# Kernel optimization log

Measured on AMD Instinct MI355X. Metric: run time of the kernel, lower is better.

The kernel has to match this reference:

```python
import jax, jax.numpy as jnp
import numpy as np

B, D, H, W = 32, 64, 64, 64
K = 1024

def setup_inputs() -> dict:
    key = jax.random.key(0)
    k1, k2 = jax.random.split(key)
    x = jax.random.normal(k1, (B, D, H, W), dtype=jnp.float32)
    # nn.Parameter(torch.rand(embeddings_dim, num_embeddings)) -> uniform [0,1)
    emb = jax.random.uniform(k2, (D, K), dtype=jnp.float32)
    return {"x": x, "emb": emb}


def reference(x, emb):
    # x: [B, D, H, W], emb: [D, K]
    b, d, h, w = x.shape
    xf = jnp.transpose(x, (0, 2, 3, 1)).reshape(-1, d)  # [N, D], N = B*H*W
    # squared L2 distance (same argmin as torch.norm(.,2) distance)
    d2 = (
        jnp.sum(xf * xf, axis=-1, keepdims=True)
        - 2.0 * (xf @ emb)
        + jnp.sum(emb * emb, axis=0)
    )  # [N, K]
    argmin = jnp.argmin(d2, axis=-1)  # [N]
    # gather codebook vectors: emb.T[argmin] -> [N, D]
    q = jnp.take(emb.T, argmin, axis=0)
    result = jnp.transpose(q.reshape(b, h, w, d), (0, 3, 1, 2))  # [B, D, H, W]
    return result, argmin.reshape(b, h, w)
```

## Files before the change

kernel.cpp:

```cpp
#include <hip/hip_runtime.h>


using half8 = __attribute__((ext_vector_type(8))) _Float16;
using half4 = __attribute__((ext_vector_type(4))) _Float16;
using f32x4 = __attribute__((ext_vector_type(4))) float;

#define XPITCH 72

__global__ void prep_kernel(const float* __restrict__ emb,
                            float* __restrict__ e2,
                            _Float16* __restrict__ eTh,
                            _Float16* __restrict__ eTl) {
    int k = blockIdx.x * 64 + threadIdx.x;
    float s = 0.f;
#pragma unroll
    for (int c = 0; c < 8; ++c) {
        half8 hv, lv;
#pragma unroll
        for (int j = 0; j < 8; ++j) {
            float v = emb[(c * 8 + j) * 1024 + k];
            s = fmaf(v, v, s);
            _Float16 h = (_Float16)v;
            hv[j] = h;
            lv[j] = (_Float16)(v - (float)h);
        }
        *(half8*)(eTh + k * 64 + c * 8) = hv;
        *(half8*)(eTl + k * 64 + c * 8) = lv;
    }
    e2[k] = s;
}

__launch_bounds__(256)
__global__ void vq_kernel(const float* __restrict__ x,
                          const _Float16* __restrict__ eTh,
                          const _Float16* __restrict__ eTl,
                          const float* __restrict__ e2,
                          const float* __restrict__ emb,
                          float* __restrict__ outq,
                          float* __restrict__ outidx) {
    __shared__ _Float16 sxh[64 * XPITCH];
    __shared__ _Float16 sxl[64 * XPITCH];
    __shared__ float rbest[256];
    __shared__ int   ridx[256];
    __shared__ int   samin[64];

    const int tx = threadIdx.x;
    const int n0 = blockIdx.x * 64;
    const int bb = n0 >> 12;
    const int hw = n0 & 4095;
    const float* xbase = x + bb * 262144 + hw;

    {
        const int p  = tx & 63;
        const int dg = (tx >> 6) << 2;
#pragma unroll
        for (int it = 0; it < 4; ++it) {
            int d0 = it * 16 + dg;
            float v0 = xbase[(d0 + 0) * 4096 + p];
            float v1 = xbase[(d0 + 1) * 4096 + p];
            float v2 = xbase[(d0 + 2) * 4096 + p];
            float v3 = xbase[(d0 + 3) * 4096 + p];
            _Float16 h0 = (_Float16)v0, h1 = (_Float16)v1,
                     h2 = (_Float16)v2, h3 = (_Float16)v3;
            half4 hv = {h0, h1, h2, h3};
            half4 lv = {(_Float16)(v0 - (float)h0), (_Float16)(v1 - (float)h1),
                        (_Float16)(v2 - (float)h2), (_Float16)(v3 - (float)h3)};
            *(half4*)(sxh + p * XPITCH + d0) = hv;
            *(half4*)(sxl + p * XPITCH + d0) = lv;
        }
    }
    __syncthreads();

    const int lane = tx & 63;
    const int w    = tx >> 6;
    const int r16  = lane & 15;
    const int q    = lane >> 4;

    half8 ah[4][2], al[4][2];
#pragma unroll
    for (int mt = 0; mt < 4; ++mt)
#pragma unroll
        for (int s = 0; s < 2; ++s) {
            ah[mt][s] = *(const half8*)(sxh + (mt * 16 + r16) * XPITCH + s * 32 + q * 8);
            al[mt][s] = *(const half8*)(sxl + (mt * 16 + r16) * XPITCH + s * 32 + q * 8);
        }
#pragma unroll
    for (int mt = 0; mt < 4; ++mt)
#pragma unroll
        for (int s = 0; s < 2; ++s) {
            asm volatile("" : "+v"(ah[mt][s]));
            asm volatile("" : "+v"(al[mt][s]));
        }

    float best[16];
    int   bestk[16];
#pragma unroll
    for (int i = 0; i < 16; ++i) { best[i] = 3.4e38f; bestk[i] = 0; }

    const int kw = w << 8;
    const _Float16* bhbase = eTh + (kw + r16) * 64 + q * 8;
    const _Float16* blbase = eTl + (kw + r16) * 64 + q * 8;
    const float*    e2base = e2 + kw + r16;

    half8 pbh0, pbh1, pbl0, pbl1; float pe2;
    half8 qbh0, qbh1, qbl0, qbl1; float qe2;

#define LOADSET(BH0, BH1, BL0, BL1, E2V, TT)                                  \
    {                                                                         \
        const int off_ = (TT) << 10;                \
        BH0 = *(const half8*)(bhbase + off_);                                 \
        BH1 = *(const half8*)(bhbase + off_ + 32);                            \
        BL0 = *(const half8*)(blbase + off_);                                 \
        BL1 = *(const half8*)(blbase + off_ + 32);                            \
        E2V = e2base[(TT) << 4];                                              \
    }

#define COMPUTE(BH0, BH1, BL0, BL1, E2V, TT)                                  \
    {                                                                         \
        const int klc_ = kw + ((TT) << 4) + r16;                              \
        _Pragma("unroll")                                                     \
        for (int mt = 0; mt < 4; ++mt) {                                      \
            f32x4 a = {0.f, 0.f, 0.f, 0.f};                                   \
            a = __builtin_amdgcn_mfma_f32_16x16x32_f16(al[mt][0], BL0, a, 0, 0, 0); \
            a = __builtin_amdgcn_mfma_f32_16x16x32_f16(al[mt][1], BL1, a, 0, 0, 0); \
            a = __builtin_amdgcn_mfma_f32_16x16x32_f16(al[mt][0], BH0, a, 0, 0, 0); \
            a = __builtin_amdgcn_mfma_f32_16x16x32_f16(al[mt][1], BH1, a, 0, 0, 0); \
            a = __builtin_amdgcn_mfma_f32_16x16x32_f16(ah[mt][0], BL0, a, 0, 0, 0); \
            a = __builtin_amdgcn_mfma_f32_16x16x32_f16(ah[mt][1], BL1, a, 0, 0, 0); \
            a = __builtin_amdgcn_mfma_f32_16x16x32_f16(ah[mt][0], BH0, a, 0, 0, 0); \
            a = __builtin_amdgcn_mfma_f32_16x16x32_f16(ah[mt][1], BH1, a, 0, 0, 0); \
            _Pragma("unroll")                                                 \
            for (int rr = 0; rr < 4; ++rr) {                                  \
                float dist_ = fmaf(-2.f, a[rr], E2V);                         \
                int i_ = mt * 4 + rr;                                         \
                if (dist_ < best[i_]) { best[i_] = dist_; bestk[i_] = klc_; } \
            }                                                                 \
        }                                                                     \
    }

    LOADSET(pbh0, pbh1, pbl0, pbl1, pe2, 0);
#pragma unroll 1
    for (int t = 0; t < 16; t += 2) {
        LOADSET(qbh0, qbh1, qbl0, qbl1, qe2, t + 1);
        COMPUTE(pbh0, pbh1, pbl0, pbl1, pe2, t);
        LOADSET(pbh0, pbh1, pbl0, pbl1, pe2, (t + 2) & 15);
        COMPUTE(qbh0, qbh1, qbl0, qbl1, qe2, t + 1);
    }

#pragma unroll
    for (int i = 0; i < 16; ++i) {
        float bv = best[i];
        int   bk = bestk[i];
#pragma unroll
        for (int m = 1; m < 16; m <<= 1) {
            float ov = __shfl_xor(bv, m, 64);
            int   ok = __shfl_xor(bk, m, 64);
            if (ov < bv || (ov == bv && ok < bk)) { bv = ov; bk = ok; }
        }
        best[i] = bv;
        bestk[i] = bk;
    }
    if (r16 == 0) {
#pragma unroll
        for (int mt = 0; mt < 4; ++mt)
#pragma unroll
            for (int rr = 0; rr < 4; ++rr) {
                int p = mt * 16 + q * 4 + rr;
                rbest[w * 64 + p] = best[mt * 4 + rr];
                ridx[w * 64 + p]  = bestk[mt * 4 + rr];
            }
    }
    __syncthreads();

    if (tx < 64) {
        float bv = rbest[tx];
        int   bk = ridx[tx];
#pragma unroll
        for (int g = 1; g < 4; ++g) {
            float v  = rbest[g * 64 + tx];
            int   kk = ridx[g * 64 + tx];
            if (v < bv || (v == bv && kk < bk)) { bv = v; bk = kk; }
        }
        samin[tx] = bk;
        outidx[n0 + tx] = (float)bk;
    }
    __syncthreads();

    const int p = tx & 63;
    const int drow = tx >> 6;
    const int amin = samin[p];
    float* obase = outq + bb * 262144 + hw + p;
#pragma unroll
    for (int it = 0; it < 16; ++it) {
        int d = (it << 2) + drow;
        obase[d * 4096] = emb[d * 1024 + amin];
    }
}

extern "C" void kernel_launch(void* const* d_in, const int* in_sizes, int n_in,
                              void* d_out, int out_size, void* d_ws, size_t ws_size,
                              hipStream_t stream) {
    const float* x   = (const float*)d_in[0];
    const float* emb = (const float*)d_in[1];
    float* outq   = (float*)d_out;
    float* outidx = outq + 8388608;

    float*    e2  = (float*)d_ws;
    _Float16* eTh = (_Float16*)((char*)d_ws + 4096);
    _Float16* eTl = (_Float16*)((char*)d_ws + 4096 + 131072);

    prep_kernel<<<16, 64, 0, stream>>>(emb, e2, eTh, eTl);
    vq_kernel<<<2048, 256, 0, stream>>>(x, eTh, eTl, e2, emb, outq, outidx);
}
```

Measured before the change: 161.2 us.

## Split VQ block across 8 waves in a 2x4 pixel-by-codebook grid

The main kernel grows to 512 threads per block. The 8 waves are split as 2 pixel halves by 4 codebook quarters, so each wave handles 32 pixels instead of 64. This halves per-wave MFMA work and register use (best arrays, A fragments), and with launch_bounds(512,4) the aim is more latency hiding. The prep kernel also uses 256 threads, splitting the fp16 hi/lo conversion across waves. The trade-off is that each B fragment loaded from global memory now feeds only half as many MFMAs, which doubles codebook read traffic per block.

After: 226.0 us. +40.1%, slower.

```diff
diff --git a/kernel.cpp b/kernel.cpp
--- a/kernel.cpp
+++ b/kernel.cpp
@@ -11,15 +11,16 @@
                             float* __restrict__ e2,
                             _Float16* __restrict__ eTh,
                             _Float16* __restrict__ eTl) {
-    int k = blockIdx.x * 64 + threadIdx.x;
-    float s = 0.f;
-#pragma unroll
-    for (int c = 0; c < 8; ++c) {
+    const int tx = threadIdx.x;
+    const int k  = blockIdx.x * 64 + (tx & 63);
+    const int cg = tx >> 6;
+#pragma unroll
+    for (int cc = 0; cc < 2; ++cc) {
+        const int c = cg + cc * 4;
         half8 hv, lv;
 #pragma unroll
         for (int j = 0; j < 8; ++j) {
             float v = emb[(c * 8 + j) * 1024 + k];
-            s = fmaf(v, v, s);
             _Float16 h = (_Float16)v;
             hv[j] = h;
             lv[j] = (_Float16)(v - (float)h);
@@ -27,10 +28,18 @@
         *(half8*)(eTh + k * 64 + c * 8) = hv;
         *(half8*)(eTl + k * 64 + c * 8) = lv;
     }
-    e2[k] = s;
+    if (cg == 0) {
+        float s = 0.f;
+#pragma unroll
+        for (int d = 0; d < 64; ++d) {
+            float v = emb[d * 1024 + k];
+            s = fmaf(v, v, s);
+        }
+        e2[k] = s;
+    }
 }
 
-__launch_bounds__(256)
+__launch_bounds__(512, 4)
 __global__ void vq_kernel(const float* __restrict__ x,
                           const _Float16* __restrict__ eTh,
                           const _Float16* __restrict__ eTl,
@@ -40,8 +49,8 @@
                           float* __restrict__ outidx) {
     __shared__ _Float16 sxh[64 * XPITCH];
     __shared__ _Float16 sxl[64 * XPITCH];
-    __shared__ float rbest[256];
-    __shared__ int   ridx[256];
+    __shared__ float rbest[8 * 32];
+    __shared__ int   ridx[8 * 32];
     __shared__ int   samin[64];
 
     const int tx = threadIdx.x;
@@ -50,54 +59,57 @@
     const int hw = n0 & 4095;
     const float* xbase = x + bb * 262144 + hw;
 
-    {
-        const int p  = tx & 63;
-        const int dg = (tx >> 6) << 2;
-#pragma unroll
-        for (int it = 0; it < 4; ++it) {
-            int d0 = it * 16 + dg;
-            float v0 = xbase[(d0 + 0) * 4096 + p];
-            float v1 = xbase[(d0 + 1) * 4096 + p];
-            float v2 = xbase[(d0 + 2) * 4096 + p];
-            float v3 = xbase[(d0 + 3) * 4096 + p];
-            _Float16 h0 = (_Float16)v0, h1 = (_Float16)v1,
-                     h2 = (_Float16)v2, h3 = (_Float16)v3;
-            half4 hv = {h0, h1, h2, h3};
-            half4 lv = {(_Float16)(v0 - (float)h0), (_Float16)(v1 - (float)h1),
-                        (_Float16)(v2 - (float)h2), (_Float16)(v3 - (float)h3)};
-            *(half4*)(sxh + p * XPITCH + d0) = hv;
-            *(half4*)(sxl + p * XPITCH + d0) = lv;
-        }
+#pragma unroll
+    for (int it = 0; it < 2; ++it) {
+        int i  = it * 512 + tx;
+        int p  = i & 63;
+        int d0 = (i >> 6) << 2;
+        float v0 = xbase[(d0 + 0) * 4096 + p];
+        float v1 = xbase[(d0 + 1) * 4096 + p];
+        float v2 = xbase[(d0 + 2) * 4096 + p];
+        float v3 = xbase[(d0 + 3) * 4096 + p];
+        _Float16 h0 = (_Float16)v0, h1 = (_Float16)v1,
+                 h2 = (_Float16)v2, h3 = (_Float16)v3;
+        half4 hv = {h0, h1, h2, h3};
+        half4 lv = {(_Float16)(v0 - (float)h0), (_Float16)(v1 - (float)h1),
+                    (_Float16)(v2 - (float)h2), (_Float16)(v3 - (float)h3)};
+        *(half4*)(sxh + p * XPITCH + d0) = hv;
+        *(half4*)(sxl + p * XPITCH + d0) = lv;
     }
     __syncthreads();
 
     const int lane = tx & 63;
     const int w    = tx >> 6;
+    const int mi   = w >> 2;
+    const int ki   = w & 3;
     const int r16  = lane & 15;
     const int q    = lane >> 4;
 
-    half8 ah[4][2], al[4][2];
-#pragma unroll
-    for (int mt = 0; mt < 4; ++mt)
+    half8 ah[2][2], al[2][2];
+#pragma unroll
+    for (int mt = 0; mt < 2; ++mt)
 #pragma unroll
         for (int s = 0; s < 2; ++s) {
-            ah[mt][s] = *(const half8*)(sxh + (mt * 16 + r16) * XPITCH + s * 32 + q * 8);
-            al[mt][s] = *(const half8*)(sxl + (mt * 16 + r16) * XPITCH + s * 32 + q * 8);
-        }
-#pragma unroll
-    for (int mt = 0; mt < 4; ++mt)
+            const int px = mi * 32 + mt * 16 + r16;
+            ah[mt][s] = *(const half8*)(sxh + px * XPITCH + s * 32 + q * 8);
+            al[mt][s] = *(const half8*)(sxl + px * XPITCH + s * 32 + q * 8);
+        }
+#pragma unroll
+    for (int mt = 0; mt < 2; ++mt)
 #pragma unroll
         for (int s = 0; s < 2; ++s) {
             asm volatile("" : "+v"(ah[mt][s]));
             asm volatile("" : "+v"(al[mt][s]));
         }
 
-    float best[16];
-    int   bestk[16];
-#pragma unroll
-    for (int i = 0; i < 16; ++i) { best[i] = 3.4e38f; bestk[i] = 0; }
-
-    const int kw = w << 8;
+    float best[8];
+    int   bestk[8];
+#pragma unroll
+    for (int i = 0; i < 8; ++i) { best[i] = 3.4e38f; bestk[i] = 0; }
+
+    const f32x4 zero4 = {0.f, 0.f, 0.f, 0.f};
+
+    const int kw = ki << 8;
     const _Float16* bhbase = eTh + (kw + r16) * 64 + q * 8;
     const _Float16* blbase = eTl + (kw + r16) * 64 + q * 8;
     const float*    e2base = e2 + kw + r16;
@@ -119,8 +131,8 @@
     {                                                                         \
         const int klc_ = kw + ((TT) << 4) + r16;                              \
         _Pragma("unroll")                                                     \
-        for (int mt = 0; mt < 4; ++mt) {                                      \
-            f32x4 a = {0.f, 0.f, 0.f, 0.f};                                   \
+        for (int mt = 0; mt < 2; ++mt) {                                      \
+            f32x4 a = zero4;                                                  \
             a = __builtin_amdgcn_mfma_f32_16x16x32_f16(al[mt][0], BL0, a, 0, 0, 0); \
             a = __builtin_amdgcn_mfma_f32_16x16x32_f16(al[mt][1], BL1, a, 0, 0, 0); \
             a = __builtin_amdgcn_mfma_f32_16x16x32_f16(al[mt][0], BH0, a, 0, 0, 0); \
@@ -148,7 +160,7 @@
     }
 
 #pragma unroll
-    for (int i = 0; i < 16; ++i) {
+    for (int i = 0; i < 8; ++i) {
         float bv = best[i];
         int   bk = bestk[i];
 #pragma unroll
@@ -162,23 +174,25 @@
     }
     if (r16 == 0) {
 #pragma unroll
-        for (int mt = 0; mt < 4; ++mt)
+        for (int mt = 0; mt < 2; ++mt)
 #pragma unroll
             for (int rr = 0; rr < 4; ++rr) {
-                int p = mt * 16 + q * 4 + rr;
-                rbest[w * 64 + p] = best[mt * 4 + rr];
-                ridx[w * 64 + p]  = bestk[mt * 4 + rr];
+                int pxl = mt * 16 + q * 4 + rr;
+                rbest[w * 32 + pxl] = best[mt * 4 + rr];
+                ridx[w * 32 + pxl]  = bestk[mt * 4 + rr];
             }
     }
     __syncthreads();
 
     if (tx < 64) {
-        float bv = rbest[tx];
-        int   bk = ridx[tx];
+        const int pmi  = tx >> 5;
+        const int pxl  = tx & 31;
+        float bv = rbest[(pmi * 4 + 0) * 32 + pxl];
+        int   bk = ridx[(pmi * 4 + 0) * 32 + pxl];
 #pragma unroll
         for (int g = 1; g < 4; ++g) {
-            float v  = rbest[g * 64 + tx];
-            int   kk = ridx[g * 64 + tx];
+            float v  = rbest[(pmi * 4 + g) * 32 + pxl];
+            int   kk = ridx[(pmi * 4 + g) * 32 + pxl];
             if (v < bv || (v == bv && kk < bk)) { bv = v; bk = kk; }
         }
         samin[tx] = bk;
@@ -191,8 +205,8 @@
     const int amin = samin[p];
     float* obase = outq + bb * 262144 + hw + p;
 #pragma unroll
-    for (int it = 0; it < 16; ++it) {
-        int d = (it << 2) + drow;
+    for (int it = 0; it < 8; ++it) {
+        int d = it * 8 + drow;
         obase[d * 4096] = emb[d * 1024 + amin];
     }
 }
@@ -209,6 +223,6 @@
     _Float16* eTh = (_Float16*)((char*)d_ws + 4096);
     _Float16* eTl = (_Float16*)((char*)d_ws + 4096 + 131072);
 
-    prep_kernel<<<16, 64, 0, stream>>>(emb, e2, eTh, eTl);
-    vq_kernel<<<2048, 256, 0, stream>>>(x, eTh, eTl, e2, emb, outq, outidx);
+    prep_kernel<<<16, 256, 0, stream>>>(emb, e2, eTh, eTl);
+    vq_kernel<<<2048, 512, 0, stream>>>(x, eTh, eTl, e2, emb, outq, outidx);
 }
```
